# Kernel optimization log

Measured on AMD Instinct MI355X. Metric: run time of the kernel, lower is better.

## Reference

```python
import jax, jax.numpy as jnp
import numpy as np

W_RESOURCE = 100.0  # init_kwargs Resource


def setup_inputs() -> dict:
    key = jax.random.key(0)
    k1, k2 = jax.random.split(key)
    B, K = 32, 2048
    values = jax.random.uniform(k1, (B, K), dtype=jnp.float32)   # >= 0 per assert
    weights = jax.random.uniform(k2, (B, K), dtype=jnp.float32)
    return {"values": values, "weights": weights}


def reference(values, weights):
    # Better_j_than_i[b, i, j] = 1.0 if values[b, j] >= values[b, i]
    v = jax.lax.stop_gradient(values)  # torch .detach()
    better = (v[:, None, :] - v[:, :, None] >= 0).astype(weights.dtype)  # [B,K,K]
    # load[b, i] = sum_j better[b,i,j] * weights[b,j]
    load = jnp.einsum('bij,bj->bi', better, weights)
    satisfying = (W_RESOURCE - load >= 0).astype(weights.dtype)  # [B,K] 0/1 mask
    return satisfying * weights
```

## Files before the change

kernel.cpp:

```cpp
#include <hip/hip_runtime.h>

#define KDIM 2048
#define BDIM 32
#define W_RESOURCE 100.0f
#define CHUNKS 8
#define SLICES 4

__global__ __launch_bounds__(1024) void alloc_kernel(const float* __restrict__ values,
                                                     const float* __restrict__ weights,
                                                     float* __restrict__ out) {
    __shared__ float sv[KDIM];
    __shared__ float sw[KDIM];
    __shared__ float part[SLICES][256];

    const int b     = blockIdx.x >> 3;
    const int chunk = blockIdx.x & 7;
    const int tid   = threadIdx.x;

    const float4* v4 = reinterpret_cast<const float4*>(values + (size_t)b * KDIM);
    const float4* w4 = reinterpret_cast<const float4*>(weights + (size_t)b * KDIM);
    float4* sv4 = reinterpret_cast<float4*>(sv);
    float4* sw4 = reinterpret_cast<float4*>(sw);
    if (tid < KDIM / 4) {
        sv4[tid] = v4[tid];
    } else {
        sw4[tid - KDIM / 4] = w4[tid - KDIM / 4];
    }
    __syncthreads();

    const int i_local = tid & 255;
    const int slice   = tid >> 8;
    const int i       = chunk * 256 + i_local;
    const float vi    = sv[i];

    const int j4_begin = slice * (KDIM / 4 / SLICES);
    const int j4_end   = j4_begin + (KDIM / 4 / SLICES);

    float acc = 0.0f;
    #pragma unroll 4
    for (int j4 = j4_begin; j4 < j4_end; ++j4) {
        float4 vj = sv4[j4];
        float4 wj = sw4[j4];
        acc += (vj.x >= vi) ? wj.x : 0.0f;
        acc += (vj.y >= vi) ? wj.y : 0.0f;
        acc += (vj.z >= vi) ? wj.z : 0.0f;
        acc += (vj.w >= vi) ? wj.w : 0.0f;
    }

    part[slice][i_local] = acc;
    __syncthreads();

    if (slice == 0) {
        float load = part[0][i_local] + part[1][i_local] + part[2][i_local] + part[3][i_local];
        out[(size_t)b * KDIM + i] = (W_RESOURCE - load >= 0.0f) ? sw[i] : 0.0f;
    }
}

extern "C" void kernel_launch(void* const* d_in, const int* in_sizes, int n_in,
                              void* d_out, int out_size, void* d_ws, size_t ws_size,
                              hipStream_t stream) {
    const float* values  = (const float*)d_in[0];
    const float* weights = (const float*)d_in[1];
    float* out = (float*)d_out;

    dim3 grid(BDIM * CHUNKS);
    dim3 block(1024);
    alloc_kernel<<<grid, block, 0, stream>>>(values, weights, out);
}
```

Baseline: 16.14 us.

## Register-block four rows per thread to reuse LDS loads across comparisons

```diff
diff --git a/kernel.cpp b/kernel.cpp
--- a/kernel.cpp
+++ b/kernel.cpp
@@ -4,7 +4,8 @@
 #define BDIM 32
 #define W_RESOURCE 100.0f
 #define CHUNKS 8
-#define SLICES 4
+#define SLICES 16
+#define G 4
 
 __global__ __launch_bounds__(1024) void alloc_kernel(const float* __restrict__ values,
                                                      const float* __restrict__ weights,
@@ -28,31 +29,46 @@
     }
     __syncthreads();
 
-    const int i_local = tid & 255;
-    const int slice   = tid >> 8;
-    const int i       = chunk * 256 + i_local;
-    const float vi    = sv[i];
+    const int lane  = tid & 63;
+    const int slice = tid >> 6;
+
+    float vi[G], acc[G];
+    #pragma unroll
+    for (int g = 0; g < G; ++g) {
+        vi[g]  = sv[chunk * 256 + g * 64 + lane];
+        acc[g] = 0.0f;
+    }
 
     const int j4_begin = slice * (KDIM / 4 / SLICES);
-    const int j4_end   = j4_begin + (KDIM / 4 / SLICES);
 
-    float acc = 0.0f;
-    #pragma unroll 4
-    for (int j4 = j4_begin; j4 < j4_end; ++j4) {
+    #pragma unroll
+    for (int it = 0; it < KDIM / 4 / SLICES; ++it) {
+        const int j4 = j4_begin + it;
         float4 vj = sv4[j4];
         float4 wj = sw4[j4];
-        acc += (vj.x >= vi) ? wj.x : 0.0f;
-        acc += (vj.y >= vi) ? wj.y : 0.0f;
-        acc += (vj.z >= vi) ? wj.z : 0.0f;
-        acc += (vj.w >= vi) ? wj.w : 0.0f;
+        #pragma unroll
+        for (int g = 0; g < G; ++g) {
+            float a = acc[g];
+            a += (vj.x >= vi[g]) ? wj.x : 0.0f;
+            a += (vj.y >= vi[g]) ? wj.y : 0.0f;
+            a += (vj.z >= vi[g]) ? wj.z : 0.0f;
+            a += (vj.w >= vi[g]) ? wj.w : 0.0f;
+            acc[g] = a;
+        }
     }
 
-    part[slice][i_local] = acc;
+    #pragma unroll
+    for (int g = 0; g < G; ++g)
+        part[slice][g * 64 + lane] = acc[g];
     __syncthreads();
 
-    if (slice == 0) {
-        float load = part[0][i_local] + part[1][i_local] + part[2][i_local] + part[3][i_local];
-        out[(size_t)b * KDIM + i] = (W_RESOURCE - load >= 0.0f) ? sw[i] : 0.0f;
+    if (tid < 256) {
+        float load = 0.0f;
+        #pragma unroll
+        for (int s = 0; s < SLICES; ++s)
+            load += part[s][tid];
+        out[(size_t)b * KDIM + chunk * 256 + tid] =
+            (W_RESOURCE - load >= 0.0f) ? sw[chunk * 256 + tid] : 0.0f;
     }
 }
 
```

Result: faster. 14.60 us (-9.5%).
